# Kernel tuning notes

Hardware: AMD Instinct MI355X
Metric: run time of the kernel (lower is better)

## Reference

```python
import jax, jax.numpy as jnp
import numpy as np

BATCH, IN_DIM, OUT_DIM, G, K = 8192, 256, 64, 64, 4
T0, T1 = 0.0, 1.0


def _bspline_basis(x, t, k):
    """Cox-de Boor recursion, vectorized over all basis indices.

    x: [B, D] evaluation points; t: [T] knot vector (non-decreasing).
    Returns basis values of order k: [B, D, T-k].
    """
    xb = x[..., None]  # [B, D, 1]
    # order-1 (degree-0) bases: indicator of half-open knot interval
    b = ((xb >= t[:-1]) & (xb < t[1:])).astype(x.dtype)  # [B, D, T-1]
    T = t.shape[0]
    for p in range(2, k + 1):
        n = T - p  # number of order-p bases
        d1 = t[p - 1:p - 1 + n] - t[:n]          # left denominators
        d2 = t[p:p + n] - t[1:1 + n]             # right denominators
        w1 = jnp.where(d1 > 0, (xb - t[:n]) / jnp.where(d1 > 0, d1, 1.0), 0.0)
        w2 = jnp.where(d2 > 0, (t[p:p + n] - xb) / jnp.where(d2 > 0, d2, 1.0), 0.0)
        b = w1 * b[..., :n] + w2 * b[..., 1:n + 1]
    return b  # [B, D, T-k]


def setup_inputs() -> dict:
    key = jax.random.key(0)
    kx, kw = jax.random.split(key)
    x = jax.random.uniform(kx, (BATCH, IN_DIM), dtype=jnp.float32)
    fan_in = (G + K) * IN_DIM
    std = float(np.sqrt(2.0 / (fan_in + OUT_DIM)))  # xavier_normal_
    w = jax.random.normal(kw, (fan_in, OUT_DIM), dtype=jnp.float32) * std
    inner = jnp.linspace(T0, T1, G + 1, dtype=jnp.float32)
    t = jnp.concatenate([jnp.full((K - 1,), T0, jnp.float32), inner,
                         jnp.full((K - 1,), T1, jnp.float32)], 0)  # [G+2k-1]
    return {"x": x, "w": w, "t": t, "k": K}


def reference(x, w, t, k):
    y1 = _bspline_basis(x, t, k)                       # [B, D, G+k-1]
    y2 = jnp.concatenate([y1, jax.nn.silu(x)[..., None]], axis=2)  # [B, D, G+k]
    return y2.reshape(x.shape[0], -1) @ w              # [B, out_dim]
```

## Files before the change

kernel.cpp:

```cpp
#include <hip/hip_runtime.h>
#include <stdint.h>

#define BATCH   8192
#define IN_DIM  256
#define OUT_DIM 64
#define NROW    68
#define N_SPLIT 16
#define D_SLICE 16
#define D_STAGE 2
#define N_STAGE 8
#define M_BLK   256
#define NM      32

typedef unsigned int u32;
typedef float f32x4 __attribute__((ext_vector_type(4)));
typedef u32   u32x2 __attribute__((ext_vector_type(2)));
typedef __bf16 bf16x2 __attribute__((ext_vector_type(2)));

#if defined(__has_builtin)
#  if __has_builtin(__builtin_amdgcn_fdot2_f32_bf16)
#    define HAVE_DOT2 1
#  endif
#endif
#ifndef HAVE_DOT2
#  define HAVE_DOT2 0
#endif

__device__ __forceinline__ u32 f2bf(float f) {
    u32 u = __float_as_uint(f);
    u += 0x7FFFu + ((u >> 16) & 1u);
    return u >> 16;
}
__device__ __forceinline__ float bflo(u32 u) { return __uint_as_float(u << 16); }
__device__ __forceinline__ float bfhi(u32 u) { return __uint_as_float(u & 0xFFFF0000u); }

__device__ __forceinline__ u32 pkbf(float lo, float hi) {
    bf16x2 v = { (__bf16)lo, (__bf16)hi };
    u32 u;
    __builtin_memcpy(&u, &v, 4);
    return u;
}

__device__ __forceinline__ float dot2bf(u32 a, u32 b, float c) {
#if HAVE_DOT2
    bf16x2 av, bv;
    __builtin_memcpy(&av, &a, 4);
    __builtin_memcpy(&bv, &b, 4);
    return __builtin_amdgcn_fdot2_f32_bf16(av, bv, c, false);
#else
    return fmaf(bflo(a), bflo(b), fmaf(bfhi(a), bfhi(b), c));
#endif
}

__device__ __forceinline__ float knotf(int i) {
    return fminf(1.f, fmaxf(0.f, (float)(i - 3) * 0.015625f));
}

__device__ __forceinline__ void make_record(float x, u32 rec[4]) {
    int s = (int)floorf(x * 64.f);
    s = max(0, min(63, s));
    const int m = s + 3;
    float N0 = 1.f, N1, N2, N3;
    const float l1 = x - knotf(m);
    const float r1 = knotf(m + 1) - x;
    {
        float tmp = N0 / (r1 + l1);
        N0 = r1 * tmp;
        N1 = l1 * tmp;
    }
    const float l2 = x - knotf(m - 1);
    const float r2 = knotf(m + 2) - x;
    {
        float tmp = N0 / (r1 + l2);
        N0 = r1 * tmp;
        float saved = l2 * tmp;
        tmp = N1 / (r2 + l1);
        N1 = saved + r2 * tmp;
        N2 = l1 * tmp;
    }
    const float l3 = x - knotf(m - 2);
    const float r3 = knotf(m + 3) - x;
    {
        float tmp = N0 / (r1 + l3);
        N0 = r1 * tmp;
        float saved = l3 * tmp;
        tmp = N1 / (r2 + l2);
        N1 = saved + r2 * tmp;
        saved = l2 * tmp;
        tmp = N2 / (r3 + l1);
        N2 = saved + r3 * tmp;
        N3 = l1 * tmp;
    }
    const float silu = x / (1.f + __expf(-x));
    rec[0] = f2bf(N0) | (f2bf(N1) << 16);
    rec[1] = f2bf(N2) | (f2bf(N3) << 16);
    rec[2] = __float_as_uint(silu);
    rec[3] = (u32)s;
}

#define TAB_D     16896
#define SILU_OFF  33792
#define REC_OFF   34304
#define LDS_U4    2656

__global__ __launch_bounds__(512, 3)
void kan_main(const float* __restrict__ X, const float* __restrict__ W,
              void* __restrict__ outbuf, int useAtomic) {
    __shared__ uint4 smem4[LDS_U4];
    char* sm = (char*)smem4;

    const int mb  = blockIdx.x;
    const int sp  = blockIdx.y;
    const int tid = threadIdx.x;
    const int r0  = mb * M_BLK;
    const int d0  = sp * D_SLICE;

    const int lane = tid & 63;
    const int wv   = tid >> 6;
    const int sub  = lane & 7;
    const int g    = lane >> 3;
    const int rb   = wv * 32;

    float acc[4][8];
#pragma unroll
    for (int t = 0; t < 4; ++t)
#pragma unroll
        for (int k = 0; k < 8; ++k) acc[t][k] = 0.f;

    for (int st = 0; st < N_STAGE; ++st) {
        const int ds = d0 + st * D_STAGE;
        __syncthreads();

        {
            const float* wbase = W + (size_t)ds * (NROW * OUT_DIM);
            for (int i = tid; i < 2 * 66 * 16; i += 512) {
                const int dl  = (i >= 1056) ? 1 : 0;
                const int rem = i - dl * 1056;
                const int r   = rem >> 4;
                const int c16 = rem & 15;
                const float* p = wbase + (size_t)dl * (NROW * OUT_DIM)
                               + r * OUT_DIM + (c16 << 2);
                float4 va = *(const float4*)p;
                float4 vb = *(const float4*)(p + OUT_DIM);
                const int byte = dl * TAB_D + r * 256 + (c16 << 4);
                *(uint4*)(sm + byte) = make_uint4(pkbf(va.x, vb.x), pkbf(va.y, vb.y),
                                                  pkbf(va.z, vb.z), pkbf(va.w, vb.w));
            }
            if (tid >= 448) {
                const int j = tid - 448;
#pragma unroll
                for (int dl = 0; dl < 2; ++dl) {
                    *(float*)(sm + SILU_OFF + dl * 256 + j * 4) =
                        wbase[(size_t)dl * (NROW * OUT_DIM) + 67 * OUT_DIM + j];
                }
            }
        }
        {
            const int r  = tid & 255;
            const int dh = tid >> 8;
            const float x = X[(size_t)(r0 + r) * IN_DIM + ds + dh];
            u32 rec[4];
            make_record(x, rec);
            *(uint4*)(sm + REC_OFF + ((dh * 256 + r) << 4)) =
                make_uint4(rec[0], rec[1], rec[2], rec[3]);
        }
        __syncthreads();

#pragma unroll
        for (int dl = 0; dl < D_STAGE; ++dl) {
            const int tb = dl * TAB_D;
            const f32x4 w67a = *(const f32x4*)(sm + SILU_OFF + dl * 256 + sub * 16);
            const f32x4 w67b = *(const f32x4*)(sm + SILU_OFF + dl * 256 + 128 + sub * 16);
#pragma unroll
            for (int t = 0; t < 4; ++t) {
                const uint4 rec = *(const uint4*)(sm + REC_OFF +
                                                  ((dl * 256 + rb + t * 8 + g) << 4));
                const u32 c01 = rec.x, c23 = rec.y;
                const float silu = __uint_as_float(rec.z);
                const int s = (int)rec.w;
                const char* r1 = sm + tb + s * 256 + sub * 16;
                const char* r2 = sm + tb + (s + 2) * 256 + sub * 16;
                const uint4 p1  = *(const uint4*)(r1);
                const uint4 p1b = *(const uint4*)(r1 + 128);
                const uint4 p2  = *(const uint4*)(r2);
                const uint4 p2b = *(const uint4*)(r2 + 128);
                acc[t][0] = dot2bf(c23, p2.x,  dot2bf(c01, p1.x,  acc[t][0]));
                acc[t][1] = dot2bf(c23, p2.y,  dot2bf(c01, p1.y,  acc[t][1]));
                acc[t][2] = dot2bf(c23, p2.z,  dot2bf(c01, p1.z,  acc[t][2]));
                acc[t][3] = dot2bf(c23, p2.w,  dot2bf(c01, p1.w,  acc[t][3]));
                acc[t][4] = dot2bf(c23, p2b.x, dot2bf(c01, p1b.x, acc[t][4]));
                acc[t][5] = dot2bf(c23, p2b.y, dot2bf(c01, p1b.y, acc[t][5]));
                acc[t][6] = dot2bf(c23, p2b.z, dot2bf(c01, p1b.z, acc[t][6]));
                acc[t][7] = dot2bf(c23, p2b.w, dot2bf(c01, p1b.w, acc[t][7]));
                acc[t][0] = fmaf(silu, w67a.x, acc[t][0]);
                acc[t][1] = fmaf(silu, w67a.y, acc[t][1]);
                acc[t][2] = fmaf(silu, w67a.z, acc[t][2]);
                acc[t][3] = fmaf(silu, w67a.w, acc[t][3]);
                acc[t][4] = fmaf(silu, w67b.x, acc[t][4]);
                acc[t][5] = fmaf(silu, w67b.y, acc[t][5]);
                acc[t][6] = fmaf(silu, w67b.z, acc[t][6]);
                acc[t][7] = fmaf(silu, w67b.w, acc[t][7]);
            }
        }
    }

    if (!useAtomic) {
        char* wsp = (char*)outbuf + (size_t)sp * (BATCH * OUT_DIM * 2);
#pragma unroll
        for (int t = 0; t < 4; ++t) {
            const int R = r0 + rb + t * 8 + g;
            u32x2 lo = { pkbf(acc[t][0], acc[t][1]), pkbf(acc[t][2], acc[t][3]) };
            u32x2 hi = { pkbf(acc[t][4], acc[t][5]), pkbf(acc[t][6], acc[t][7]) };
            __builtin_nontemporal_store(lo, (u32x2*)(wsp + (size_t)R * 128 + sub * 8));
            __builtin_nontemporal_store(hi, (u32x2*)(wsp + (size_t)R * 128 + 64 + sub * 8));
        }
    } else {
        float* out = (float*)outbuf;
#pragma unroll
        for (int t = 0; t < 4; ++t) {
            const int R = r0 + rb + t * 8 + g;
#pragma unroll
            for (int k = 0; k < 4; ++k) {
                atomicAdd(out + (size_t)R * 64 + sub * 4 + k, acc[t][k]);
                atomicAdd(out + (size_t)R * 64 + 32 + sub * 4 + k, acc[t][k + 4]);
            }
        }
    }
}

__global__ __launch_bounds__(256)
void kan_reduce(const u32* __restrict__ ws, float* __restrict__ out) {
    const int i = blockIdx.x * 256 + threadIdx.x;
    const u32x2* w2 = (const u32x2*)ws;
    float a0 = 0.f, a1 = 0.f, a2 = 0.f, a3 = 0.f;
#pragma unroll
    for (int s = 0; s < N_SPLIT; ++s) {
        u32x2 v = __builtin_nontemporal_load(
            &w2[(size_t)s * (BATCH * OUT_DIM / 4) + i]);
        a0 += bflo(v.x); a1 += bfhi(v.x);
        a2 += bflo(v.y); a3 += bfhi(v.y);
    }
    f32x4 r = { a0, a1, a2, a3 };
    *(f32x4*)(out + (size_t)i * 4) = r;
}

extern "C" void kernel_launch(void* const* d_in, const int* in_sizes, int n_in,
                              void* d_out, int out_size, void* d_ws, size_t ws_size,
                              hipStream_t stream) {
    const float* X = (const float*)d_in[0];
    const float* W = (const float*)d_in[1];
    float* out = (float*)d_out;
    const size_t need = (size_t)N_SPLIT * BATCH * OUT_DIM * 2;
    dim3 grid(NM, N_SPLIT);
    if (ws_size >= need) {
        kan_main<<<grid, 512, 0, stream>>>(X, W, d_ws, 0);
        kan_reduce<<<(BATCH * OUT_DIM / 4) / 256, 256, 0, stream>>>((const u32*)d_ws, out);
    } else {
        (void)hipMemsetAsync(d_out, 0, (size_t)out_size * sizeof(float), stream);
        kan_main<<<grid, 512, 0, stream>>>(X, W, d_out, 1);
    }
}
```

Before: 49.20 us.

## Double-buffer LDS stages with register prefetch of next input dim

```diff
diff --git a/kernel.cpp b/kernel.cpp
--- a/kernel.cpp
+++ b/kernel.cpp
@@ -7,8 +7,7 @@
 #define NROW    68
 #define N_SPLIT 16
 #define D_SLICE 16
-#define D_STAGE 2
-#define N_STAGE 8
+#define N_STAGE 16
 #define M_BLK   256
 #define NM      32
 
@@ -98,12 +97,13 @@
     rec[3] = (u32)s;
 }
 
-#define TAB_D     16896
-#define SILU_OFF  33792
-#define REC_OFF   34304
-#define LDS_U4    2656
-
-__global__ __launch_bounds__(512, 3)
+#define TAB_OFF    0
+#define SILU_OFF   16896
+#define REC_OFF    17152
+#define BUF_STRIDE 21248
+#define LDS_U4     2656
+
+__global__ __launch_bounds__(512, 4)
 void kan_main(const float* __restrict__ X, const float* __restrict__ W,
               void* __restrict__ outbuf, int useAtomic) {
     __shared__ uint4 smem4[LDS_U4];
@@ -121,86 +121,100 @@
     const int g    = lane >> 3;
     const int rb   = wv * 32;
 
+    const int c16 = tid & 15;
+    const int e0r = tid >> 4;
+    const int e1r = e0r + 32;
+    const int e2r = e0r + 64;
+
+    float4 va0, vb0, va1, vb1, va2, vb2;
+    float xreg = 0.f, sreg = 0.f;
+
+#define LOAD_REGS(DS) do {                                                     \
+        const float* wb_ = W + (size_t)(DS) * (NROW * OUT_DIM);                \
+        const float* p0_ = wb_ + e0r * OUT_DIM + c16 * 4;                      \
+        va0 = *(const float4*)p0_;  vb0 = *(const float4*)(p0_ + OUT_DIM);     \
+        const float* p1_ = wb_ + e1r * OUT_DIM + c16 * 4;                      \
+        va1 = *(const float4*)p1_;  vb1 = *(const float4*)(p1_ + OUT_DIM);     \
+        if (tid < 32) {                                                        \
+            const float* p2_ = wb_ + e2r * OUT_DIM + c16 * 4;                  \
+            va2 = *(const float4*)p2_;  vb2 = *(const float4*)(p2_ + OUT_DIM); \
+        }                                                                      \
+        if (tid >= 448) sreg = wb_[67 * OUT_DIM + (tid - 448)];                \
+        if (tid < 256)  xreg = X[(size_t)(r0 + tid) * IN_DIM + (DS)];          \
+    } while (0)
+
+#define WRITE_STAGE(BN) do {                                                   \
+        char* b_ = (BN);                                                       \
+        *(uint4*)(b_ + TAB_OFF + e0r * 256 + c16 * 16) =                       \
+            make_uint4(pkbf(va0.x, vb0.x), pkbf(va0.y, vb0.y),                 \
+                       pkbf(va0.z, vb0.z), pkbf(va0.w, vb0.w));                \
+        *(uint4*)(b_ + TAB_OFF + e1r * 256 + c16 * 16) =                       \
+            make_uint4(pkbf(va1.x, vb1.x), pkbf(va1.y, vb1.y),                 \
+                       pkbf(va1.z, vb1.z), pkbf(va1.w, vb1.w));                \
+        if (tid < 32)                                                          \
+            *(uint4*)(b_ + TAB_OFF + e2r * 256 + c16 * 16) =                   \
+                make_uint4(pkbf(va2.x, vb2.x), pkbf(va2.y, vb2.y),             \
+                           pkbf(va2.z, vb2.z), pkbf(va2.w, vb2.w));            \
+        if (tid >= 448) *(float*)(b_ + SILU_OFF + (tid - 448) * 4) = sreg;     \
+        if (tid < 256) {                                                       \
+            u32 rec_[4];                                                       \
+            make_record(xreg, rec_);                                           \
+            *(uint4*)(b_ + REC_OFF + (tid << 4)) =                             \
+                make_uint4(rec_[0], rec_[1], rec_[2], rec_[3]);                \
+        }                                                                      \
+    } while (0)
+
     float acc[4][8];
 #pragma unroll
     for (int t = 0; t < 4; ++t)
 #pragma unroll
         for (int k = 0; k < 8; ++k) acc[t][k] = 0.f;
 
+    LOAD_REGS(d0);
+    WRITE_STAGE(sm);
+    __syncthreads();
+    LOAD_REGS(d0 + 1);
+
     for (int st = 0; st < N_STAGE; ++st) {
-        const int ds = d0 + st * D_STAGE;
-        __syncthreads();
-
-        {
-            const float* wbase = W + (size_t)ds * (NROW * OUT_DIM);
-            for (int i = tid; i < 2 * 66 * 16; i += 512) {
-                const int dl  = (i >= 1056) ? 1 : 0;
-                const int rem = i - dl * 1056;
-                const int r   = rem >> 4;
-                const int c16 = rem & 15;
-                const float* p = wbase + (size_t)dl * (NROW * OUT_DIM)
-                               + r * OUT_DIM + (c16 << 2);
-                float4 va = *(const float4*)p;
-                float4 vb = *(const float4*)(p + OUT_DIM);
-                const int byte = dl * TAB_D + r * 256 + (c16 << 4);
-                *(uint4*)(sm + byte) = make_uint4(pkbf(va.x, vb.x), pkbf(va.y, vb.y),
-                                                  pkbf(va.z, vb.z), pkbf(va.w, vb.w));
-            }
-            if (tid >= 448) {
-                const int j = tid - 448;
-#pragma unroll
-                for (int dl = 0; dl < 2; ++dl) {
-                    *(float*)(sm + SILU_OFF + dl * 256 + j * 4) =
-                        wbase[(size_t)dl * (NROW * OUT_DIM) + 67 * OUT_DIM + j];
-                }
-            }
-        }
-        {
-            const int r  = tid & 255;
-            const int dh = tid >> 8;
-            const float x = X[(size_t)(r0 + r) * IN_DIM + ds + dh];
-            u32 rec[4];
-            make_record(x, rec);
-            *(uint4*)(sm + REC_OFF + ((dh * 256 + r) << 4)) =
-                make_uint4(rec[0], rec[1], rec[2], rec[3]);
-        }
-        __syncthreads();
-
-#pragma unroll
-        for (int dl = 0; dl < D_STAGE; ++dl) {
-            const int tb = dl * TAB_D;
-            const f32x4 w67a = *(const f32x4*)(sm + SILU_OFF + dl * 256 + sub * 16);
-            const f32x4 w67b = *(const f32x4*)(sm + SILU_OFF + dl * 256 + 128 + sub * 16);
-#pragma unroll
-            for (int t = 0; t < 4; ++t) {
-                const uint4 rec = *(const uint4*)(sm + REC_OFF +
-                                                  ((dl * 256 + rb + t * 8 + g) << 4));
-                const u32 c01 = rec.x, c23 = rec.y;
-                const float silu = __uint_as_float(rec.z);
-                const int s = (int)rec.w;
-                const char* r1 = sm + tb + s * 256 + sub * 16;
-                const char* r2 = sm + tb + (s + 2) * 256 + sub * 16;
-                const uint4 p1  = *(const uint4*)(r1);
-                const uint4 p1b = *(const uint4*)(r1 + 128);
-                const uint4 p2  = *(const uint4*)(r2);
-                const uint4 p2b = *(const uint4*)(r2 + 128);
-                acc[t][0] = dot2bf(c23, p2.x,  dot2bf(c01, p1.x,  acc[t][0]));
-                acc[t][1] = dot2bf(c23, p2.y,  dot2bf(c01, p1.y,  acc[t][1]));
-                acc[t][2] = dot2bf(c23, p2.z,  dot2bf(c01, p1.z,  acc[t][2]));
-                acc[t][3] = dot2bf(c23, p2.w,  dot2bf(c01, p1.w,  acc[t][3]));
-                acc[t][4] = dot2bf(c23, p2b.x, dot2bf(c01, p1b.x, acc[t][4]));
-                acc[t][5] = dot2bf(c23, p2b.y, dot2bf(c01, p1b.y, acc[t][5]));
-                acc[t][6] = dot2bf(c23, p2b.z, dot2bf(c01, p1b.z, acc[t][6]));
-                acc[t][7] = dot2bf(c23, p2b.w, dot2bf(c01, p1b.w, acc[t][7]));
-                acc[t][0] = fmaf(silu, w67a.x, acc[t][0]);
-                acc[t][1] = fmaf(silu, w67a.y, acc[t][1]);
-                acc[t][2] = fmaf(silu, w67a.z, acc[t][2]);
-                acc[t][3] = fmaf(silu, w67a.w, acc[t][3]);
-                acc[t][4] = fmaf(silu, w67b.x, acc[t][4]);
-                acc[t][5] = fmaf(silu, w67b.y, acc[t][5]);
-                acc[t][6] = fmaf(silu, w67b.z, acc[t][6]);
-                acc[t][7] = fmaf(silu, w67b.w, acc[t][7]);
-            }
+        char* bc = sm + (st & 1) * BUF_STRIDE;
+        char* bn = sm + ((st & 1) ^ 1) * BUF_STRIDE;
+
+        const f32x4 w67a = *(const f32x4*)(bc + SILU_OFF + sub * 16);
+        const f32x4 w67b = *(const f32x4*)(bc + SILU_OFF + 128 + sub * 16);
+#pragma unroll
+        for (int t = 0; t < 4; ++t) {
+            const uint4 rec = *(const uint4*)(bc + REC_OFF + ((rb + t * 8 + g) << 4));
+            const u32 c01 = rec.x, c23 = rec.y;
+            const float silu = __uint_as_float(rec.z);
+            const int s = (int)rec.w;
+            const char* r1 = bc + TAB_OFF + s * 256 + sub * 16;
+            const char* r2 = bc + TAB_OFF + (s + 2) * 256 + sub * 16;
+            const uint4 p1  = *(const uint4*)(r1);
+            const uint4 p1b = *(const uint4*)(r1 + 128);
+            const uint4 p2  = *(const uint4*)(r2);
+            const uint4 p2b = *(const uint4*)(r2 + 128);
+            acc[t][0] = dot2bf(c23, p2.x,  dot2bf(c01, p1.x,  acc[t][0]));
+            acc[t][1] = dot2bf(c23, p2.y,  dot2bf(c01, p1.y,  acc[t][1]));
+            acc[t][2] = dot2bf(c23, p2.z,  dot2bf(c01, p1.z,  acc[t][2]));
+            acc[t][3] = dot2bf(c23, p2.w,  dot2bf(c01, p1.w,  acc[t][3]));
+            acc[t][4] = dot2bf(c23, p2b.x, dot2bf(c01, p1b.x, acc[t][4]));
+            acc[t][5] = dot2bf(c23, p2b.y, dot2bf(c01, p1b.y, acc[t][5]));
+            acc[t][6] = dot2bf(c23, p2b.z, dot2bf(c01, p1b.z, acc[t][6]));
+            acc[t][7] = dot2bf(c23, p2b.w, dot2bf(c01, p1b.w, acc[t][7]));
+            acc[t][0] = fmaf(silu, w67a.x, acc[t][0]);
+            acc[t][1] = fmaf(silu, w67a.y, acc[t][1]);
+            acc[t][2] = fmaf(silu, w67a.z, acc[t][2]);
+            acc[t][3] = fmaf(silu, w67a.w, acc[t][3]);
+            acc[t][4] = fmaf(silu, w67b.x, acc[t][4]);
+            acc[t][5] = fmaf(silu, w67b.y, acc[t][5]);
+            acc[t][6] = fmaf(silu, w67b.z, acc[t][6]);
+            acc[t][7] = fmaf(silu, w67b.w, acc[t][7]);
+        }
+
+        if (st < N_STAGE - 1) {
+            WRITE_STAGE(bn);
+            __syncthreads();
+            if (st < N_STAGE - 2) LOAD_REGS(d0 + st + 2);
         }
     }
 
@@ -226,6 +240,8 @@
             }
         }
     }
+#undef LOAD_REGS
+#undef WRITE_STAGE
 }
 
 __global__ __launch_bounds__(256)
```

New measurement: 173.2 us. +252.0%, slower.
